# Kernel optimization log

Measured on AMD Instinct MI355X. Metric: run time of the kernel, lower is better.

Reference implementation:

```python
import jax, jax.numpy as jnp
import numpy as np

D = 128          # feature / hidden dim
K = 3            # SortPooling k (hard-coded in Topkpool)
NUM_CLASS = 10
EPS = 1e-5       # BatchNorm eps


def setup_inputs() -> dict:
    key = jax.random.key(0)
    ks = jax.random.split(key, 24)
    G, NPG = 512, 200
    N = G * NPG
    E = 1638400
    inp = {
        "x": jax.random.normal(ks[0], (N, D), jnp.float32),
        "src": jax.random.randint(ks[1], (E,), 0, N),
        "dst": jax.random.randint(ks[2], (E,), 0, N),
        "num_graphs": G,
        "nodes_per_graph": NPG,
    }
    s = 1.0 / np.sqrt(D)
    for i in (1, 2, 3):
        inp[f"W{i}"] = jax.random.uniform(ks[2 + i], (D, D), jnp.float32, -s, s)
        inp[f"b{i}"] = jnp.zeros((D,), jnp.float32)
        inp[f"g{i}"] = jnp.ones((D,), jnp.float32)   # BN gamma
        inp[f"bt{i}"] = jnp.zeros((D,), jnp.float32)  # BN beta
    sp = 1.0 / np.sqrt(K * D)
    for i in range(4):
        inp[f"P{i}w"] = jax.random.uniform(ks[10 + i], (K * D, NUM_CLASS), jnp.float32, -sp, sp)
        inp[f"P{i}b"] = jnp.zeros((NUM_CLASS,), jnp.float32)
    return inp


def _graph_conv(h, src, dst, W, b, n):
    # DGL GraphConv, norm='both': D_in^{-1/2} A (D_out^{-1/2} h) W + b
    one = jnp.ones((src.shape[0],), h.dtype)
    deg_out = jnp.zeros((n,), h.dtype).at[src].add(one)
    deg_in = jnp.zeros((n,), h.dtype).at[dst].add(one)
    h = h * jax.lax.rsqrt(jnp.maximum(deg_out, 1.0))[:, None]
    agg = jax.ops.segment_sum(h[src], dst, num_segments=n)  # [N, D] scatter-add
    agg = agg * jax.lax.rsqrt(jnp.maximum(deg_in, 1.0))[:, None]
    return agg @ W + b


def _bn_relu(h, g, bt):
    mu = h.mean(axis=0)
    var = jnp.mean((h - mu) ** 2, axis=0)  # biased var, torch BN training mode
    return jax.nn.relu((h - mu) * jax.lax.rsqrt(var + EPS) * g + bt)


def _sort_pool(h, G, npg):
    # DGL SortPooling: sort each node's feature vector ascending, then pick
    # top-K nodes per graph by last (max) channel, concatenate features.
    d = h.shape[-1]
    hs = jnp.sort(h, axis=-1).reshape(G, npg, d)
    idx = jax.lax.top_k(hs[:, :, -1], K)[1]                       # [G, K]
    return jnp.take_along_axis(hs, idx[:, :, None], axis=1).reshape(G, K * d)


def reference(x, W1, b1, g1, bt1, W2, b2, g2, bt2, W3, b3, g3, bt3,
              P0w, P0b, P1w, P1b, P2w, P2b, P3w, P3b,
              src, dst, num_graphs, nodes_per_graph):
    n = x.shape[0]
    reps = [x]
    h = x
    for W, b, g, bt in ((W1, b1, g1, bt1), (W2, b2, g2, bt2), (W3, b3, g3, bt3)):
        h = _bn_relu(_graph_conv(h, src, dst, W, b, n), g, bt)
        reps.append(h)
    score = jnp.zeros((num_graphs, NUM_CLASS), x.dtype)
    for h_i, Pw, Pb in zip(reps, (P0w, P1w, P2w, P3w), (P0b, P1b, P2b, P3b)):
        score = score + _sort_pool(h_i, num_graphs, nodes_per_graph) @ Pw + Pb
    return score
```

## Files before the change

### kernel.cpp

```cpp
#include <hip/hip_runtime.h>
#include <hip/hip_bf16.h>

#define D 128
#define KTOP 3
#define NCLS 10
#define EPS 1e-5f
#define GBM 128
#define BCAP 64


__global__ __launch_bounds__(256) void prologue_kernel(
        const int* __restrict__ src,
        int* __restrict__ deg_out, int E,
        const float* __restrict__ x, float* __restrict__ nodemax, int N,
        float* __restrict__ score, const float* __restrict__ pb0,
        const float* __restrict__ pb1, const float* __restrict__ pb2,
        const float* __restrict__ pb3, int G) {
    int b = blockIdx.x;
    int nbDeg = (E + 255) >> 8;
    if (b < 8 * nbDeg) {
        int xcd = b & 7;
        int e = (b >> 3) * 256 + threadIdx.x;
        int lo = xcd * (N >> 3), hi = lo + (N >> 3);
        if (e < E) {
            int s = src[e];
            if (s >= lo && s < hi) atomicAdd(&deg_out[s], 1);
        }
        return;
    }
    b -= 8 * nbDeg;
    int nbR = N >> 3;
    if (b < nbR) {
        int node = b * 8 + (threadIdx.x >> 5);
        int l = threadIdx.x & 31;
        float4 v = *reinterpret_cast<const float4*>(x + (size_t)node * D + 4 * l);
        float m = fmaxf(fmaxf(v.x, v.y), fmaxf(v.z, v.w));
#pragma unroll
        for (int d = 16; d > 0; d >>= 1) m = fmaxf(m, __shfl_xor(m, d, 64));
        if (l == 0) nodemax[node] = m;
        return;
    }
    for (int i = threadIdx.x; i < G * NCLS; i += 256) {
        int c = i % NCLS;
        score[i] = pb0[c] + pb1[c] + pb2[c] + pb3[c];
    }
}


__global__ __launch_bounds__(256) void csr_scatter(
        const int* __restrict__ src, const int* __restrict__ dst,
        const int* __restrict__ deg_out,
        int* __restrict__ cursor, int2* __restrict__ csrw, int E, int N) {
    int b = blockIdx.x;
    int xcd = b & 7;
    int e = (b >> 3) * 256 + threadIdx.x;
    if (e >= E) return;
    int d = dst[e];
    int lo = xcd * (N >> 3), hi = lo + (N >> 3);
    if (d < lo || d >= hi) return;
    int s = src[e];
    int slot = atomicAdd(&cursor[d], 1);
    if (slot >= BCAP) return;
    int dg = deg_out[s]; if (dg < 1) dg = 1;
    int2 p; p.x = s; p.y = __float_as_int(rsqrtf((float)dg));
    csrw[(size_t)d * BCAP + slot] = p;
}

__global__ void pad_kernel(const int* __restrict__ cursor, int2* __restrict__ csrw, int N) {
    int d = blockIdx.x * blockDim.x + threadIdx.x;
    if (d >= N) return;
    int c = cursor[d]; if (c > BCAP) c = BCAP;
    int end = (c + 7) & ~7;
    int2 z; z.x = 0; z.y = 0;
    for (int i = c; i < end; ++i) csrw[(size_t)d * BCAP + i] = z;
}

__device__ __forceinline__ float4 bnrelu4(float4 v, float4 sc, float4 sh) {
    float4 r;
    r.x = fmaxf(fmaf(v.x, sc.x, sh.x), 0.f);
    r.y = fmaxf(fmaf(v.y, sc.y, sh.y), 0.f);
    r.z = fmaxf(fmaf(v.z, sc.z, sh.z), 0.f);
    r.w = fmaxf(fmaf(v.w, sc.w, sh.w), 0.f);
    return r;
}


__global__ __launch_bounds__(256) void aggregate_head(
        const float* __restrict__ hin, const int* __restrict__ cursor,
        const int2* __restrict__ csrw, float* __restrict__ hout, int nAgg,
        const float* __restrict__ nodemax, const float* __restrict__ Pw,
        float* __restrict__ score, int NPG,
        const float* __restrict__ bns, const float* __restrict__ g,
        const float* __restrict__ bt, float invN) {
    __shared__ float ov[256];
    __shared__ float sv[256];
    __shared__ int   si[256];
    __shared__ int   sel[KTOP];
    __shared__ float sbuf[KTOP][D];
    __shared__ float red[4][NCLS];
    __shared__ float scs[D], shs[D];
    int b = blockIdx.x;
    int t = threadIdx.x;
    bool useBN = (bns != nullptr);
    if (useBN) {
        if (t < D) {
            float mu  = bns[t] * invN;
            float var = bns[D + t] * invN - mu * mu;
            float inv = rsqrtf(var + EPS);
            float s = g[t] * inv;
            scs[t] = s;
            shs[t] = bt[t] - mu * s;
        }
        __syncthreads();
    }
    if (b < nAgg) {
        int node = b * 8 + (t >> 5);
        int l = t & 31;
        int deg = cursor[node];
        int end = (deg + 7) & ~7; if (end > BCAP) end = BCAP;
        const int2* bkt = csrw + (size_t)node * BCAP;
        const float* base = hin + 4 * l;
        float4 sc4, sh4;
        if (useBN) {
            sc4 = *reinterpret_cast<const float4*>(&scs[4 * l]);
            sh4 = *reinterpret_cast<const float4*>(&shs[4 * l]);
        }
        float4 a0 = {0.f, 0.f, 0.f, 0.f}, a1 = a0;
        for (int e = 0; e < end; e += 8) {
            const int4* ce = reinterpret_cast<const int4*>(bkt + e);
            int4 p0 = ce[0], p1 = ce[1], p2 = ce[2], p3 = ce[3];
            float4 v0 = *reinterpret_cast<const float4*>(base + (size_t)p0.x * D);
            float4 v1 = *reinterpret_cast<const float4*>(base + (size_t)p0.z * D);
            float4 v2 = *reinterpret_cast<const float4*>(base + (size_t)p1.x * D);
            float4 v3 = *reinterpret_cast<const float4*>(base + (size_t)p1.z * D);
            float4 v4 = *reinterpret_cast<const float4*>(base + (size_t)p2.x * D);
            float4 v5 = *reinterpret_cast<const float4*>(base + (size_t)p2.z * D);
            float4 v6 = *reinterpret_cast<const float4*>(base + (size_t)p3.x * D);
            float4 v7 = *reinterpret_cast<const float4*>(base + (size_t)p3.z * D);
            if (useBN) {
                v0 = bnrelu4(v0, sc4, sh4); v1 = bnrelu4(v1, sc4, sh4);
                v2 = bnrelu4(v2, sc4, sh4); v3 = bnrelu4(v3, sc4, sh4);
                v4 = bnrelu4(v4, sc4, sh4); v5 = bnrelu4(v5, sc4, sh4);
                v6 = bnrelu4(v6, sc4, sh4); v7 = bnrelu4(v7, sc4, sh4);
            }
            float w0 = __int_as_float(p0.y), w1 = __int_as_float(p0.w);
            float w2 = __int_as_float(p1.y), w3 = __int_as_float(p1.w);
            float w4 = __int_as_float(p2.y), w5 = __int_as_float(p2.w);
            float w6 = __int_as_float(p3.y), w7 = __int_as_float(p3.w);
            a0.x += w0*v0.x; a0.y += w0*v0.y; a0.z += w0*v0.z; a0.w += w0*v0.w;
            a1.x += w1*v1.x; a1.y += w1*v1.y; a1.z += w1*v1.z; a1.w += w1*v1.w;
            a0.x += w2*v2.x; a0.y += w2*v2.y; a0.z += w2*v2.z; a0.w += w2*v2.w;
            a1.x += w3*v3.x; a1.y += w3*v3.y; a1.z += w3*v3.z; a1.w += w3*v3.w;
            a0.x += w4*v4.x; a0.y += w4*v4.y; a0.z += w4*v4.z; a0.w += w4*v4.w;
            a1.x += w5*v5.x; a1.y += w5*v5.y; a1.z += w5*v5.z; a1.w += w5*v5.w;
            a0.x += w6*v6.x; a0.y += w6*v6.y; a0.z += w6*v6.z; a0.w += w6*v6.w;
            a1.x += w7*v7.x; a1.y += w7*v7.y; a1.z += w7*v7.z; a1.w += w7*v7.w;
        }
        float ri = rsqrtf((float)(deg < 1 ? 1 : deg));
        float4 r;
        r.x = (a0.x + a1.x) * ri;
        r.y = (a0.y + a1.y) * ri;
        r.z = (a0.z + a1.z) * ri;
        r.w = (a0.w + a1.w) * ri;
        *reinterpret_cast<float4*>(hout + (size_t)node * D + 4 * l) = r;
        return;
    }

    int gr = b - nAgg;
    ov[t] = (t < NPG) ? nodemax[(size_t)gr * NPG + t] : -3.4e38f;
    __syncthreads();
    for (int ks = 0; ks < KTOP; ++ks) {
        sv[t] = ov[t]; si[t] = t;
        __syncthreads();
        for (int s = 128; s > 0; s >>= 1) {
            if (t < s) {
                float a = sv[t], c = sv[t + s];
                int ia = si[t], ib = si[t + s];
                if (c > a || (c == a && ib < ia)) { sv[t] = c; si[t] = ib; }
            }
            __syncthreads();
        }
        if (t == 0) { sel[ks] = si[0]; ov[si[0]] = -3.4e38f; }
        __syncthreads();
    }
    int u = t >> 7, tl = t & 127;
    {
        float v = hin[((size_t)gr * NPG + sel[u]) * D + tl];
        sbuf[u][tl] = useBN ? fmaxf(fmaf(v, scs[tl], shs[tl]), 0.f) : v;
        if (t < 128) {
            float v2 = hin[((size_t)gr * NPG + sel[2]) * D + t];
            sbuf[2][t] = useBN ? fmaxf(fmaf(v2, scs[t], shs[t]), 0.f) : v2;
        }
    }
    __syncthreads();
    for (int size = 2; size <= D; size <<= 1) {
        for (int stride = size >> 1; stride > 0; stride >>= 1) {
            int ixj = tl ^ stride;
            if (ixj > tl) {
                float a = sbuf[u][tl], c = sbuf[u][ixj];
                bool up = ((tl & size) == 0);
                if ((a > c) == up) { sbuf[u][tl] = c; sbuf[u][ixj] = a; }
            }
            if (t < 128) {
                int ix2 = t ^ stride;
                if (ix2 > t) {
                    float a = sbuf[2][t], c = sbuf[2][ix2];
                    bool up = ((t & size) == 0);
                    if ((a > c) == up) { sbuf[2][t] = c; sbuf[2][ix2] = a; }
                }
            }
            __syncthreads();
        }
    }
    float part[NCLS];
    float v0 = sbuf[u][tl];
    const float* pw0 = Pw + (size_t)(u * D + tl) * NCLS;
#pragma unroll
    for (int c = 0; c < NCLS; ++c) part[c] = v0 * pw0[c];
    if (t < 128) {
        float v2 = sbuf[2][t];
        const float* pw2 = Pw + (size_t)(2 * D + t) * NCLS;
#pragma unroll
        for (int c = 0; c < NCLS; ++c) part[c] += v2 * pw2[c];
    }
    int lane = t & 63, wid = t >> 6;
#pragma unroll
    for (int c = 0; c < NCLS; ++c) {
        float xx = part[c];
#pragma unroll
        for (int o = 32; o > 0; o >>= 1) xx += __shfl_down(xx, o, 64);
        if (lane == 0) red[wid][c] = xx;
    }
    __syncthreads();
    if (t < NCLS)
        atomicAdd(&score[gr * NCLS + t],
                  red[0][t] + red[1][t] + red[2][t] + red[3][t]);
}


__device__ __forceinline__ void gemm_chunk(const float* __restrict__ ain, size_t rowBase,
        int kc, int c0, const float (*Wl)[D], float (&acc)[4][8]) {
    const float* ap = ain + rowBase * D + kc;
    float4 a0 = *reinterpret_cast<const float4*>(ap);
    float4 a1 = *reinterpret_cast<const float4*>(ap + D);
    float4 a2 = *reinterpret_cast<const float4*>(ap + 2 * D);
    float4 a3 = *reinterpret_cast<const float4*>(ap + 3 * D);
#pragma unroll 2
    for (int k4 = 0; k4 < 16; ++k4) {
        float4 n0 = a0, n1 = a1, n2 = a2, n3 = a3;
        if (k4 < 15) {
            const float* np = ap + 4 * (k4 + 1);
            n0 = *reinterpret_cast<const float4*>(np);
            n1 = *reinterpret_cast<const float4*>(np + D);
            n2 = *reinterpret_cast<const float4*>(np + 2 * D);
            n3 = *reinterpret_cast<const float4*>(np + 3 * D);
        }
#pragma unroll
        for (int j = 0; j < 4; ++j) {
            int kk = 4 * k4 + j;
            float4 w0 = *reinterpret_cast<const float4*>(&Wl[kk][c0]);
            float4 w1 = *reinterpret_cast<const float4*>(&Wl[kk][c0 + 4]);
            float av[4];
            av[0] = (j==0)?a0.x:(j==1)?a0.y:(j==2)?a0.z:a0.w;
            av[1] = (j==0)?a1.x:(j==1)?a1.y:(j==2)?a1.z:a1.w;
            av[2] = (j==0)?a2.x:(j==1)?a2.y:(j==2)?a2.z:a2.w;
            av[3] = (j==0)?a3.x:(j==1)?a3.y:(j==2)?a3.z:a3.w;
            float wv[8] = {w0.x, w0.y, w0.z, w0.w, w1.x, w1.y, w1.z, w1.w};
#pragma unroll
            for (int i = 0; i < 4; ++i)
#pragma unroll
                for (int jj = 0; jj < 8; ++jj) acc[i][jj] += av[i] * wv[jj];
        }
        a0 = n0; a1 = n1; a2 = n2; a3 = n3;
    }
}

__global__ __launch_bounds__(512) void gemm_bn(const float* __restrict__ ain,
        const float* __restrict__ W, const float* __restrict__ bias,
        float* __restrict__ hout, float* __restrict__ bnsums, int N) {
    __shared__ __align__(16) float Wl[64][D];
    int t = threadIdx.x;
    int cg = t & 15;
    int rs = t >> 4;
    int c0 = cg * 8;
    size_t rowBase = (size_t)blockIdx.x * GBM + 4 * rs;

    float acc[4][8];
#pragma unroll
    for (int i = 0; i < 4; ++i)
#pragma unroll
        for (int j = 0; j < 8; ++j) acc[i][j] = 0.f;

    const float4* Wv = reinterpret_cast<const float4*>(W);
    float4* Wd = reinterpret_cast<float4*>(&Wl[0][0]);
    float4 wpre[4];
#pragma unroll
    for (int i = 0; i < 4; ++i) wpre[i] = Wv[t + 512 * i];
#pragma unroll
    for (int i = 0; i < 4; ++i) Wd[t + 512 * i] = wpre[i];
#pragma unroll
    for (int i = 0; i < 4; ++i) wpre[i] = Wv[2048 + t + 512 * i];
    __syncthreads();
    gemm_chunk(ain, rowBase, 0, c0, Wl, acc);
    __syncthreads();
#pragma unroll
    for (int i = 0; i < 4; ++i) Wd[t + 512 * i] = wpre[i];
    __syncthreads();
    gemm_chunk(ain, rowBase, 64, c0, Wl, acc);

    float4 b0 = *reinterpret_cast<const float4*>(&bias[c0]);
    float4 b1 = *reinterpret_cast<const float4*>(&bias[c0 + 4]);
    float bv[8] = {b0.x, b0.y, b0.z, b0.w, b1.x, b1.y, b1.z, b1.w};
    float cs[8], cq[8];
#pragma unroll
    for (int j = 0; j < 8; ++j) { cs[j] = 0.f; cq[j] = 0.f; }
#pragma unroll
    for (int i = 0; i < 4; ++i) {
#pragma unroll
        for (int j = 0; j < 8; ++j) {
            float v = acc[i][j] + bv[j];
            acc[i][j] = v;
            cs[j] += v;
            cq[j] += v * v;
        }
    }
#pragma unroll
    for (int i = 0; i < 4; ++i) {
        size_t row = rowBase + i;
        float4 o0, o1;
        o0.x = acc[i][0]; o0.y = acc[i][1]; o0.z = acc[i][2]; o0.w = acc[i][3];
        o1.x = acc[i][4]; o1.y = acc[i][5]; o1.z = acc[i][6]; o1.w = acc[i][7];
        *reinterpret_cast<float4*>(&hout[row * D + c0])     = o0;
        *reinterpret_cast<float4*>(&hout[row * D + c0 + 4]) = o1;
    }
#pragma unroll
    for (int j = 0; j < 8; ++j) {
        cs[j] += __shfl_xor(cs[j], 16, 64); cq[j] += __shfl_xor(cq[j], 16, 64);
        cs[j] += __shfl_xor(cs[j], 32, 64); cq[j] += __shfl_xor(cq[j], 32, 64);
    }
    __syncthreads();
    float* red = &Wl[0][0];
    int wid = t >> 6, lane = t & 63;
    if (lane < 16) {
#pragma unroll
        for (int j = 0; j < 8; ++j) {
            red[wid * 256 + lane * 16 + j]     = cs[j];
            red[wid * 256 + lane * 16 + 8 + j] = cq[j];
        }
    }
    __syncthreads();
    if (t < 256) {
        float s = 0.f;
#pragma unroll
        for (int w = 0; w < 8; ++w) s += red[w * 256 + t];
        int cgi = t >> 4, r = t & 15;
        int ch = cgi * 8 + (r & 7);
        atomicAdd(&bnsums[(r < 8 ? 0 : D) + ch], s);
    }
}


__global__ __launch_bounds__(256) void bn_nodemax(const float* __restrict__ h,
        const float* __restrict__ bnsums, const float* __restrict__ g,
        const float* __restrict__ bt, float* __restrict__ nodemax, int N, float invN) {
    __shared__ float sc[D], sh[D];
    int t = threadIdx.x;
    if (t < D) {
        float mu  = bnsums[t] * invN;
        float var = bnsums[D + t] * invN - mu * mu;
        float inv = rsqrtf(var + EPS);
        float s = g[t] * inv;
        sc[t] = s;
        sh[t] = bt[t] - mu * s;
    }
    __syncthreads();
    int node = (blockIdx.x * 256 + t) >> 5;
    int l = t & 31;
    if (node >= N) return;
    float4 v = *reinterpret_cast<const float4*>(h + (size_t)node * D + 4 * l);
    float4 a = *reinterpret_cast<const float4*>(&sc[4 * l]);
    float4 b = *reinterpret_cast<const float4*>(&sh[4 * l]);
    v.x = fmaxf(fmaf(v.x, a.x, b.x), 0.f);
    v.y = fmaxf(fmaf(v.y, a.y, b.y), 0.f);
    v.z = fmaxf(fmaf(v.z, a.z, b.z), 0.f);
    v.w = fmaxf(fmaf(v.w, a.w, b.w), 0.f);
    float m = fmaxf(fmaxf(v.x, v.y), fmaxf(v.z, v.w));
#pragma unroll
    for (int d = 16; d > 0; d >>= 1) m = fmaxf(m, __shfl_xor(m, d, 64));
    if (l == 0) nodemax[node] = m;
}


extern "C" void kernel_launch(void* const* d_in, const int* in_sizes, int n_in,
                              void* d_out, int out_size, void* d_ws, size_t ws_size,
                              hipStream_t stream) {
    const float* x   = (const float*)d_in[0];
    const int*   src = (const int*)d_in[1];
    const int*   dst = (const int*)d_in[2];
    const float* W[3]  = {(const float*)d_in[5],  (const float*)d_in[9],  (const float*)d_in[13]};
    const float* bb[3] = {(const float*)d_in[6],  (const float*)d_in[10], (const float*)d_in[14]};
    const float* gg[3] = {(const float*)d_in[7],  (const float*)d_in[11], (const float*)d_in[15]};
    const float* bt[3] = {(const float*)d_in[8],  (const float*)d_in[12], (const float*)d_in[16]};
    const float* Pw[4] = {(const float*)d_in[17], (const float*)d_in[19], (const float*)d_in[21], (const float*)d_in[23]};
    const float* Pb[4] = {(const float*)d_in[18], (const float*)d_in[20], (const float*)d_in[22], (const float*)d_in[24]};

    int N = in_sizes[0] / D;
    int E = in_sizes[1];
    int G = out_size / NCLS;
    int NPG = N / G;
    float* score = (float*)d_out;

    size_t NF = (size_t)N * D;
    float* fws     = (float*)d_ws;
    float* H       = fws;
    float* T       = H + NF;
    float* nodemax = T + NF;
    float* bnsums  = nodemax + N;
    int* deg_out = (int*)(bnsums + 6 * D);
    int* cursor  = deg_out + N;
    int2* csrw   = (int2*)(cursor + N);

    int nbDeg = (E + 255) >> 8;
    int nbR = N >> 3;
    float invN = 1.0f / (float)N;

    hipMemsetAsync(deg_out, 0, sizeof(int) * (size_t)2 * N, stream);
    hipMemsetAsync(bnsums, 0, sizeof(float) * 6 * D, stream);

    prologue_kernel<<<8 * nbDeg + nbR + 1, 256, 0, stream>>>(
        src, deg_out, E, x, nodemax, N,
        score, Pb[0], Pb[1], Pb[2], Pb[3], G);
    csr_scatter<<<8 * nbDeg, 256, 0, stream>>>(src, dst, deg_out, cursor, csrw, E, N);
    pad_kernel<<<(N + 255) / 256, 256, 0, stream>>>(cursor, csrw, N);

    int nAgg = N / 8;
    const float* hin = x;
    const float* curBns = nullptr;
    const float* curG = nullptr;
    const float* curBt = nullptr;
    for (int l = 0; l < 3; ++l) {
        float* bns = bnsums + l * 2 * D;
        aggregate_head<<<nAgg + G, 256, 0, stream>>>(
            hin, cursor, csrw, T, nAgg, nodemax, Pw[l], score, NPG,
            curBns, curG, curBt, invN);
        gemm_bn<<<N / GBM, 512, 0, stream>>>(T, W[l], bb[l], H, bns, N);
        bn_nodemax<<<N / 8, 256, 0, stream>>>(H, bns, gg[l], bt[l], nodemax, N, invN);
        hin = H;
        curBns = bns; curG = gg[l]; curBt = bt[l];
    }
    aggregate_head<<<G, 256, 0, stream>>>(
        H, cursor, csrw, T, 0, nodemax, Pw[3], score, NPG,
        curBns, curG, curBt, invN);
}
```

Before: 799.3 us.

## Fuse layer-0 sort-pool head into CSR scatter and use 16 destination shards

Moves the layer-0 SortPooling head (per-graph top-k selection, bitonic sort of the chosen rows, projection into score) out of the first aggregate launch and into the CSR scatter kernel. The head blocks now run alongside the scatter blocks instead of alongside the first aggregation. The scatter also changes from 8 to 16 destination shards, with each shard still mapped onto an XCD by block index. This is meant to narrow the per-block destination range for better atomic and cache locality, at the price of reading src/dst twice as many times.

```diff
diff --git a/kernel.cpp b/kernel.cpp
--- a/kernel.cpp
+++ b/kernel.cpp
@@ -47,23 +47,104 @@
 }
 
 
-__global__ __launch_bounds__(256) void csr_scatter(
+__global__ __launch_bounds__(256) void scatter_head(
         const int* __restrict__ src, const int* __restrict__ dst,
         const int* __restrict__ deg_out,
-        int* __restrict__ cursor, int2* __restrict__ csrw, int E, int N) {
+        int* __restrict__ cursor, int2* __restrict__ csrw, int E, int N, int nbDeg,
+        const float* __restrict__ x, const float* __restrict__ nodemax,
+        const float* __restrict__ Pw, float* __restrict__ score, int NPG, int G) {
+    __shared__ float ov[256];
+    __shared__ float sv[256];
+    __shared__ int   si[256];
+    __shared__ int   sel[KTOP];
+    __shared__ float sbuf[KTOP][D];
+    __shared__ float red[4][NCLS];
     int b = blockIdx.x;
-    int xcd = b & 7;
-    int e = (b >> 3) * 256 + threadIdx.x;
-    if (e >= E) return;
-    int d = dst[e];
-    int lo = xcd * (N >> 3), hi = lo + (N >> 3);
-    if (d < lo || d >= hi) return;
-    int s = src[e];
-    int slot = atomicAdd(&cursor[d], 1);
-    if (slot >= BCAP) return;
-    int dg = deg_out[s]; if (dg < 1) dg = 1;
-    int2 p; p.x = s; p.y = __float_as_int(rsqrtf((float)dg));
-    csrw[(size_t)d * BCAP + slot] = p;
+    int t = threadIdx.x;
+    if (b >= G) {
+        int bb = b - G;
+        int xcd = bb & 7;
+        int jc = bb >> 3;
+        int j = jc / nbDeg;
+        int c = jc - j * nbDeg;
+        int shard = xcd + 8 * j;
+        int e = c * 256 + t;
+        if (e >= E) return;
+        int d = dst[e];
+        int lo = shard * (N >> 4), hi = lo + (N >> 4);
+        if (d < lo || d >= hi) return;
+        int s = src[e];
+        int slot = atomicAdd(&cursor[d], 1);
+        if (slot >= BCAP) return;
+        int dg = deg_out[s]; if (dg < 1) dg = 1;
+        int2 p; p.x = s; p.y = __float_as_int(rsqrtf((float)dg));
+        csrw[(size_t)d * BCAP + slot] = p;
+        return;
+    }
+
+    int gr = b;
+    ov[t] = (t < NPG) ? nodemax[(size_t)gr * NPG + t] : -3.4e38f;
+    __syncthreads();
+    for (int ks = 0; ks < KTOP; ++ks) {
+        sv[t] = ov[t]; si[t] = t;
+        __syncthreads();
+        for (int s = 128; s > 0; s >>= 1) {
+            if (t < s) {
+                float a = sv[t], c = sv[t + s];
+                int ia = si[t], ib = si[t + s];
+                if (c > a || (c == a && ib < ia)) { sv[t] = c; si[t] = ib; }
+            }
+            __syncthreads();
+        }
+        if (t == 0) { sel[ks] = si[0]; ov[si[0]] = -3.4e38f; }
+        __syncthreads();
+    }
+    int u = t >> 7, tl = t & 127;
+    sbuf[u][tl] = x[((size_t)gr * NPG + sel[u]) * D + tl];
+    if (t < 128) sbuf[2][t] = x[((size_t)gr * NPG + sel[2]) * D + t];
+    __syncthreads();
+    for (int size = 2; size <= D; size <<= 1) {
+        for (int stride = size >> 1; stride > 0; stride >>= 1) {
+            int ixj = tl ^ stride;
+            if (ixj > tl) {
+                float a = sbuf[u][tl], c = sbuf[u][ixj];
+                bool up = ((tl & size) == 0);
+                if ((a > c) == up) { sbuf[u][tl] = c; sbuf[u][ixj] = a; }
+            }
+            if (t < 128) {
+                int ix2 = t ^ stride;
+                if (ix2 > t) {
+                    float a = sbuf[2][t], c = sbuf[2][ix2];
+                    bool up = ((t & size) == 0);
+                    if ((a > c) == up) { sbuf[2][t] = c; sbuf[2][ix2] = a; }
+                }
+            }
+            __syncthreads();
+        }
+    }
+    float part[NCLS];
+    float v0 = sbuf[u][tl];
+    const float* pw0 = Pw + (size_t)(u * D + tl) * NCLS;
+#pragma unroll
+    for (int c = 0; c < NCLS; ++c) part[c] = v0 * pw0[c];
+    if (t < 128) {
+        float v2 = sbuf[2][t];
+        const float* pw2 = Pw + (size_t)(2 * D + t) * NCLS;
+#pragma unroll
+        for (int c = 0; c < NCLS; ++c) part[c] += v2 * pw2[c];
+    }
+    int lane = t & 63, wid = t >> 6;
+#pragma unroll
+    for (int c = 0; c < NCLS; ++c) {
+        float xx = part[c];
+#pragma unroll
+        for (int o = 32; o > 0; o >>= 1) xx += __shfl_down(xx, o, 64);
+        if (lane == 0) red[wid][c] = xx;
+    }
+    __syncthreads();
+    if (t < NCLS)
+        atomicAdd(&score[gr * NCLS + t],
+                  red[0][t] + red[1][t] + red[2][t] + red[3][t]);
 }
 
 __global__ void pad_kernel(const int* __restrict__ cursor, int2* __restrict__ csrw, int N) {
@@ -430,7 +511,9 @@
     prologue_kernel<<<8 * nbDeg + nbR + 1, 256, 0, stream>>>(
         src, deg_out, E, x, nodemax, N,
         score, Pb[0], Pb[1], Pb[2], Pb[3], G);
-    csr_scatter<<<8 * nbDeg, 256, 0, stream>>>(src, dst, deg_out, cursor, csrw, E, N);
+    scatter_head<<<G + 16 * nbDeg, 256, 0, stream>>>(
+        src, dst, deg_out, cursor, csrw, E, N, nbDeg,
+        x, nodemax, Pw[0], score, NPG, G);
     pad_kernel<<<(N + 255) / 256, 256, 0, stream>>>(cursor, csrw, N);
 
     int nAgg = N / 8;
@@ -440,7 +523,8 @@
     const float* curBt = nullptr;
     for (int l = 0; l < 3; ++l) {
         float* bns = bnsums + l * 2 * D;
-        aggregate_head<<<nAgg + G, 256, 0, stream>>>(
+        int nHead = (l == 0) ? 0 : G;
+        aggregate_head<<<nAgg + nHead, 256, 0, stream>>>(
             hin, cursor, csrw, T, nAgg, nodemax, Pw[l], score, NPG,
             curBns, curG, curBt, invN);
         gemm_bn<<<N / GBM, 512, 0, stream>>>(T, W[l], bb[l], H, bns, N);
```

Measured after the change: 817.7 us. 2.3% more time.
